# Optimization experiments

Hardware: AMD Instinct MI355X
Metric: run time of the kernel (lower is better)

Reference implementation:

```python
import jax, jax.numpy as jnp
import numpy as np

N, L, E, H = 2, 2048, 1024, 16
D = E // H  # head_dimension


def setup_inputs() -> dict:
    key = jax.random.key(0)
    kq, kk, kv, km, kw, kb = jax.random.split(key, 6)
    return {
        "query": jax.random.normal(kq, (N, L, E), dtype=jnp.float32),
        "key": jax.random.normal(kk, (N, L, E), dtype=jnp.float32),
        "value": jax.random.normal(kv, (N, L, E), dtype=jnp.float32),
        "mask": jax.random.randint(km, (N, 1, L, L), 0, 2, dtype=jnp.int32),
        "W_out": jax.random.normal(kw, (E, E), dtype=jnp.float32) / np.float32(np.sqrt(E)),
        "b_out": jax.random.normal(kb, (E,), dtype=jnp.float32) * np.float32(0.02),
    }


def reference(query, key, value, mask, W_out, b_out):
    n, ql, e = query.shape
    # split heads: [N, L, E] -> [N, L, H, D]
    q = query.reshape(n, ql, H, D)
    k = key.reshape(n, key.shape[1], H, D)
    v = value.reshape(n, value.shape[1], H, D)
    # energy: [N, H, Q, K]
    energy = jnp.einsum('nqhd,nkhd->nhqk', q, k)
    energy = jnp.where(mask == 0, jnp.float32(-1e20), energy)
    scale = jnp.float32(E) ** jnp.float32(0.5)
    attention = jax.nn.softmax(energy / scale, axis=3)
    out = jnp.einsum('nhql,nlhd->nqhd', attention, v).reshape(n, ql, H * D)
    # fully_connected_output: torch Linear -> x @ W^T + b
    return out @ W_out.T + b_out
```

## Files before the change

kernel.cpp:

```cpp
#include <hip/hip_runtime.h>
#include <hip/hip_bf16.h>

#define N_ 2
#define L_ 2048
#define E_ 1024
#define H_ 16
#define D_ 64

typedef __attribute__((ext_vector_type(8))) short bf16x8;
typedef __attribute__((ext_vector_type(4))) short bf16x4;
typedef __attribute__((ext_vector_type(4))) float f32x4;

static __device__ __forceinline__ short bfc(float f) {
    union { __bf16 h; short s; } u;
    u.h = (__bf16)f;
    return u.s;
}

static __device__ __forceinline__ void glds16(const void* g, void* l) {
    __builtin_amdgcn_global_load_lds(
        (const __attribute__((address_space(1))) unsigned int*)g,
        (__attribute__((address_space(3))) unsigned int*)l, 16, 0, 0);
}

__global__ __launch_bounds__(256) void pack_kv(
    const float* __restrict__ K, const float* __restrict__ V,
    unsigned short* __restrict__ Kp, unsigned short* __restrict__ Vp)
{
    __shared__ short T[64][72];

    const int bx = blockIdx.x;
    const int kt = bx & 31;
    const int h  = (bx >> 5) & 15;
    const int n  = bx >> 9;
    const int tid = threadIdx.x;
    const int kq = tid >> 4, c4 = tid & 15;

    const size_t inbase = ((size_t)(n * L_) + kt * 64) * E_ + h * D_;
    const size_t obase  = ((size_t)((n * H_ + h) * 32 + kt)) * 4096;

#pragma unroll
    for (int jj = 0; jj < 4; ++jj) {
        const int r = kq + jj * 16;
        const float4 f = *reinterpret_cast<const float4*>(K + inbase + (size_t)r * E_ + c4 * 4);
        bf16x4 w;
        w[0] = bfc(f.x); w[1] = bfc(f.y); w[2] = bfc(f.z); w[3] = bfc(f.w);
        *reinterpret_cast<bf16x4*>(&Kp[obase + r * 64 + ((c4 * 4) ^ ((r & 7) << 3))]) = w;
    }
#pragma unroll
    for (int jj = 0; jj < 4; ++jj) {
        const int k = kq + jj * 16;
        const float4 f = *reinterpret_cast<const float4*>(V + inbase + (size_t)k * E_ + c4 * 4);
        T[c4 * 4 + 0][k] = bfc(f.x);
        T[c4 * 4 + 1][k] = bfc(f.y);
        T[c4 * 4 + 2][k] = bfc(f.z);
        T[c4 * 4 + 3][k] = bfc(f.w);
    }
    __syncthreads();
#pragma unroll
    for (int jj = 0; jj < 2; ++jj) {
        const int d  = (tid >> 3) + jj * 32;
        const int k8 = (tid & 7) * 8;
        const bf16x8 v = *reinterpret_cast<const bf16x8*>(&T[d][k8]);
        *reinterpret_cast<bf16x8*>(&Vp[obase + d * 64 + (k8 ^ ((d & 7) << 3))]) = v;
    }
}

__global__ __launch_bounds__(256) void pack_mask(
    const int* __restrict__ mask, unsigned long long* __restrict__ Mb)
{
    const int tid  = threadIdx.x;
    const int lane = tid & 63;
    const int wave = tid >> 6;
    const int r = blockIdx.x * 4 + wave;
    const int* src = mask + (size_t)r * L_;
    unsigned long long* dst = Mb + (size_t)r * 32;
#pragma unroll 4
    for (int kt = 0; kt < 32; ++kt) {
        const int mv = src[kt * 64 + lane];
        const unsigned long long b = __ballot(mv != 0);
        if (lane == 0) dst[kt] = b;
    }
}

__global__ __launch_bounds__(256, 4) void attn_fwd(
    const unsigned short* __restrict__ Kp, const unsigned short* __restrict__ Vp,
    const float* __restrict__ Q, const unsigned long long* __restrict__ Mb,
    unsigned short* __restrict__ Obf )
{
    __shared__ __align__(16) short K_lds[2][64 * 64];
    __shared__ __align__(16) short V_lds[2][64 * 64];
    __shared__ __align__(16) short P_lds[4][32][72];

    const int tid   = threadIdx.x;
    const int lane  = tid & 63;
    const int wave  = tid >> 6;
    const int row16 = lane & 15;
    const int g     = lane >> 4;
    const int sw    = (row16 & 7) << 3;

    const int bid = blockIdx.x;
    const int bx  = (bid & 7) * 64 + (bid >> 3);
    const int qt = bx & 15;
    const int h  = (bx >> 4) & 15;
    const int n  = bx >> 8;

    const int q0w = qt * 128 + wave * 32;

    const float SCL = 0.0450842200277801f;

    bf16x8 qa[2][2];
#pragma unroll
    for (int hq = 0; hq < 2; ++hq) {
        const float* qptr = Q + ((size_t)(n * L_ + q0w + hq * 16 + row16)) * E_ + h * D_;
#pragma unroll
        for (int c = 0; c < 2; ++c) {
            const float4 f0 = *reinterpret_cast<const float4*>(qptr + 32 * c + 8 * g);
            const float4 f1 = *reinterpret_cast<const float4*>(qptr + 32 * c + 8 * g + 4);
            bf16x8 a;
            a[0] = bfc(f0.x * SCL); a[1] = bfc(f0.y * SCL);
            a[2] = bfc(f0.z * SCL); a[3] = bfc(f0.w * SCL);
            a[4] = bfc(f1.x * SCL); a[5] = bfc(f1.y * SCL);
            a[6] = bfc(f1.z * SCL); a[7] = bfc(f1.w * SCL);
            qa[hq][c] = a;
        }
    }

    f32x4 o[2][4];
#pragma unroll
    for (int hq = 0; hq < 2; ++hq)
#pragma unroll
        for (int dt = 0; dt < 4; ++dt) {
            o[hq][dt][0] = 0.f; o[hq][dt][1] = 0.f;
            o[hq][dt][2] = 0.f; o[hq][dt][3] = 0.f;
        }
    float lrun[2] = {0.f, 0.f};

    const unsigned long long* mrow0 = Mb + ((size_t)(n * L_) + q0w + row16) * 32;
    const unsigned long long* mrow1 = mrow0 + 16 * 32;
    const char* kvb = (const char*)Kp + ((size_t)(n * H_ + h) * 32) * 8192;
    const char* vvb = (const char*)Vp + ((size_t)(n * H_ + h) * 32) * 8192;

    {
        const int off = wave * 2048;
        glds16(kvb + off + lane * 16,        (char*)&K_lds[0][0] + off);
        glds16(kvb + off + 1024 + lane * 16, (char*)&K_lds[0][0] + off + 1024);
        glds16(vvb + off + lane * 16,        (char*)&V_lds[0][0] + off);
        glds16(vvb + off + 1024 + lane * 16, (char*)&V_lds[0][0] + off + 1024);
    }
    __syncthreads();

    for (int kt = 0; kt < 32; ++kt) {
        const int cur = kt & 1;
        if (kt + 1 < 32) {
            const char* kg = kvb + (size_t)(kt + 1) * 8192;
            const char* vg = vvb + (size_t)(kt + 1) * 8192;
            const int off = wave * 2048;
            glds16(kg + off + lane * 16,        (char*)&K_lds[cur ^ 1][0] + off);
            glds16(kg + off + 1024 + lane * 16, (char*)&K_lds[cur ^ 1][0] + off + 1024);
            glds16(vg + off + lane * 16,        (char*)&V_lds[cur ^ 1][0] + off);
            glds16(vg + off + 1024 + lane * 16, (char*)&V_lds[cur ^ 1][0] + off + 1024);
        }
        const unsigned long long mb0 = mrow0[kt];
        const unsigned long long mb1 = mrow1[kt];

        f32x4 s[2][4];
#pragma unroll
        for (int t = 0; t < 4; ++t) {
            f32x4 a0, a1;
            a0[0] = 0.f; a0[1] = 0.f; a0[2] = 0.f; a0[3] = 0.f;
            a1[0] = 0.f; a1[1] = 0.f; a1[2] = 0.f; a1[3] = 0.f;
#pragma unroll
            for (int c = 0; c < 2; ++c) {
                const bf16x8 kf = *reinterpret_cast<const bf16x8*>(
                    &K_lds[cur][(t * 16 + row16) * 64 + ((32 * c + 8 * g) ^ sw)]);
                a0 = __builtin_amdgcn_mfma_f32_16x16x32_bf16(kf, qa[0][c], a0, 0, 0, 0);
                a1 = __builtin_amdgcn_mfma_f32_16x16x32_bf16(kf, qa[1][c], a1, 0, 0, 0);
            }
            s[0][t] = a0; s[1][t] = a1;
        }

#pragma unroll
        for (int hq = 0; hq < 2; ++hq) {
            const unsigned long long mb = hq ? mb1 : mb0;
            const unsigned lo = (unsigned)(mb >> (g * 4));
            const unsigned hi = (unsigned)(mb >> (32 + g * 4));
            float ps = 0.f;
#pragma unroll
            for (int t = 0; t < 4; ++t) {
                const unsigned w32 = (t < 2) ? lo : hi;
                const int base = (t & 1) * 16;
#pragma unroll
                for (int i = 0; i < 4; ++i) {
                    float p = exp2f(s[hq][t][i]);
                    p = (w32 & (1u << (base + i))) ? p : 0.0f;
                    s[hq][t][i] = p;
                    ps += p;
                }
            }
            lrun[hq] += ps;
#pragma unroll
            for (int t = 0; t < 4; ++t) {
                bf16x4 w;
                w[0] = bfc(s[hq][t][0]); w[1] = bfc(s[hq][t][1]);
                w[2] = bfc(s[hq][t][2]); w[3] = bfc(s[hq][t][3]);
                *reinterpret_cast<bf16x4*>(
                    &P_lds[wave][hq * 16 + row16][(t * 16 + g * 4) ^ sw]) = w;
            }
        }

#pragma unroll
        for (int c = 0; c < 2; ++c) {
            const bf16x8 pb0 = *reinterpret_cast<const bf16x8*>(
                &P_lds[wave][row16][(32 * c + 8 * g) ^ sw]);
            const bf16x8 pb1 = *reinterpret_cast<const bf16x8*>(
                &P_lds[wave][16 + row16][(32 * c + 8 * g) ^ sw]);
#pragma unroll
            for (int dt = 0; dt < 4; ++dt) {
                const bf16x8 va = *reinterpret_cast<const bf16x8*>(
                    &V_lds[cur][(dt * 16 + row16) * 64 + ((32 * c + 8 * g) ^ sw)]);
                o[0][dt] = __builtin_amdgcn_mfma_f32_16x16x32_bf16(va, pb0, o[0][dt], 0, 0, 0);
                o[1][dt] = __builtin_amdgcn_mfma_f32_16x16x32_bf16(va, pb1, o[1][dt], 0, 0, 0);
            }
        }

        __syncthreads();
    }

#pragma unroll
    for (int hq = 0; hq < 2; ++hq) {
        float l = lrun[hq];
        l += __shfl_xor(l, 16);
        l += __shfl_xor(l, 32);
        const float inv = 1.0f / l;
        unsigned short* ob = Obf + (size_t)(n * L_ + q0w + hq * 16 + row16) * E_ + h * D_;
#pragma unroll
        for (int dt = 0; dt < 4; ++dt) {
            bf16x4 w;
            w[0] = bfc(o[hq][dt][0] * inv); w[1] = bfc(o[hq][dt][1] * inv);
            w[2] = bfc(o[hq][dt][2] * inv); w[3] = bfc(o[hq][dt][3] * inv);
            *reinterpret_cast<bf16x4*>(&ob[(dt * 16 + g * 4) ^ sw]) = w;
        }
    }
}

__global__ __launch_bounds__(256) void attn_fwd_legacy(
    const unsigned short* __restrict__ Kp, const unsigned short* __restrict__ Vp,
    const float* __restrict__ Q, const int* __restrict__ mask,
    unsigned short* __restrict__ Obf)
{
    __shared__ __align__(16) short K_lds[64 * 64];
    __shared__ __align__(16) short V_lds[64 * 64];
    __shared__ __align__(16) short P_lds[4][16][72];

    const int tid   = threadIdx.x;
    const int lane  = tid & 63;
    const int wave  = tid >> 6;
    const int row16 = lane & 15;
    const int g     = lane >> 4;
    const int sw    = (row16 & 7) << 3;

    const int bx = blockIdx.x;
    const int qt = bx & 31;
    const int h  = (bx >> 5) & 15;
    const int n  = bx >> 9;

    const int q0w = qt * 64 + wave * 16;
    const float SCL = 0.0450842200277801f;

    const float* qptr = Q + ((size_t)(n * L_ + q0w + row16)) * E_ + h * D_;
    bf16x8 qa[2];
#pragma unroll
    for (int c = 0; c < 2; ++c) {
        const float4 f0 = *reinterpret_cast<const float4*>(qptr + 32 * c + 8 * g);
        const float4 f1 = *reinterpret_cast<const float4*>(qptr + 32 * c + 8 * g + 4);
        bf16x8 a;
        a[0] = bfc(f0.x * SCL); a[1] = bfc(f0.y * SCL);
        a[2] = bfc(f0.z * SCL); a[3] = bfc(f0.w * SCL);
        a[4] = bfc(f1.x * SCL); a[5] = bfc(f1.y * SCL);
        a[6] = bfc(f1.z * SCL); a[7] = bfc(f1.w * SCL);
        qa[c] = a;
    }

    f32x4 o[4];
#pragma unroll
    for (int dt = 0; dt < 4; ++dt) { o[dt][0] = 0.f; o[dt][1] = 0.f; o[dt][2] = 0.f; o[dt][3] = 0.f; }
    float lrun = 0.f;

    const int* mrow = mask + (size_t)n * L_ * L_ + (size_t)(q0w + row16) * L_;
    const char* kvb = (const char*)Kp + ((size_t)(n * H_ + h) * 32) * 8192;
    const char* vvb = (const char*)Vp + ((size_t)(n * H_ + h) * 32) * 8192;

    for (int kt = 0; kt < 32; ++kt) {
        int4 mv[4];
#pragma unroll
        for (int t = 0; t < 4; ++t)
            mv[t] = *reinterpret_cast<const int4*>(mrow + kt * 64 + t * 16 + g * 4);

        __syncthreads();
        {
            const char* kg = kvb + (size_t)kt * 8192;
            const char* vg = vvb + (size_t)kt * 8192;
#pragma unroll
            for (int it = 0; it < 2; ++it) {
                const int off = wave * 2048 + it * 1024;
                glds16(kg + off + lane * 16, (char*)K_lds + off);
                glds16(vg + off + lane * 16, (char*)V_lds + off);
            }
        }
        __syncthreads();

        f32x4 s[4];
#pragma unroll
        for (int t = 0; t < 4; ++t) {
            f32x4 acc; acc[0] = 0.f; acc[1] = 0.f; acc[2] = 0.f; acc[3] = 0.f;
#pragma unroll
            for (int c = 0; c < 2; ++c) {
                const bf16x8 kf = *reinterpret_cast<const bf16x8*>(
                    &K_lds[(t * 16 + row16) * 64 + ((32 * c + 8 * g) ^ sw)]);
                acc = __builtin_amdgcn_mfma_f32_16x16x32_bf16(kf, qa[c], acc, 0, 0, 0);
            }
            s[t] = acc;
        }
#pragma unroll
        for (int t = 0; t < 4; ++t) {
            s[t][0] = mv[t].x ? s[t][0] : -3.0e18f;
            s[t][1] = mv[t].y ? s[t][1] : -3.0e18f;
            s[t][2] = mv[t].z ? s[t][2] : -3.0e18f;
            s[t][3] = mv[t].w ? s[t][3] : -3.0e18f;
        }
        float ps = 0.f;
#pragma unroll
        for (int t = 0; t < 4; ++t) {
            const float p0 = exp2f(s[t][0]);
            const float p1 = exp2f(s[t][1]);
            const float p2 = exp2f(s[t][2]);
            const float p3 = exp2f(s[t][3]);
            s[t][0] = p0; s[t][1] = p1; s[t][2] = p2; s[t][3] = p3;
            ps += (p0 + p1) + (p2 + p3);
        }
        lrun += ps;
#pragma unroll
        for (int t = 0; t < 4; ++t) {
            bf16x4 w;
            w[0] = bfc(s[t][0]); w[1] = bfc(s[t][1]);
            w[2] = bfc(s[t][2]); w[3] = bfc(s[t][3]);
            *reinterpret_cast<bf16x4*>(&P_lds[wave][row16][t * 16 + g * 4]) = w;
        }
#pragma unroll
        for (int c = 0; c < 2; ++c) {
            const bf16x8 pb = *reinterpret_cast<const bf16x8*>(
                &P_lds[wave][row16][32 * c + 8 * g]);
#pragma unroll
            for (int dt = 0; dt < 4; ++dt) {
                const bf16x8 va = *reinterpret_cast<const bf16x8*>(
                    &V_lds[(dt * 16 + row16) * 64 + ((32 * c + 8 * g) ^ sw)]);
                o[dt] = __builtin_amdgcn_mfma_f32_16x16x32_bf16(va, pb, o[dt], 0, 0, 0);
            }
        }
    }

    float l = lrun;
    l += __shfl_xor(l, 16);
    l += __shfl_xor(l, 32);
    const float inv = 1.0f / l;
    unsigned short* ob = Obf + (size_t)(n * L_ + q0w + row16) * E_ + h * D_;
#pragma unroll
    for (int dt = 0; dt < 4; ++dt) {
        bf16x4 w;
        w[0] = bfc(o[dt][0] * inv); w[1] = bfc(o[dt][1] * inv);
        w[2] = bfc(o[dt][2] * inv); w[3] = bfc(o[dt][3] * inv);
        *reinterpret_cast<bf16x4*>(&ob[(dt * 16 + g * 4) ^ sw]) = w;
    }
}

__global__ __launch_bounds__(256) void convert_w(
    const float* __restrict__ W, unsigned short* __restrict__ Wb)
{
    const int i = (blockIdx.x * 256 + threadIdx.x) * 4;
    const int row = i >> 10, col = i & 1023;
    const float4 f = *reinterpret_cast<const float4*>(W + i);
    bf16x4 w;
    w[0] = bfc(f.x); w[1] = bfc(f.y); w[2] = bfc(f.z); w[3] = bfc(f.w);
    const int ch = col & ~63, incol = col & 63;
    *reinterpret_cast<bf16x4*>(&Wb[row * 1024 + ch + (incol ^ ((row & 7) << 3))]) = w;
}

__global__ __launch_bounds__(256) void out_proj_bf(
    const unsigned short* __restrict__ A,
    const unsigned short* __restrict__ Wb,
    const float* __restrict__ bias, float* __restrict__ Cout)
{
    __shared__ __align__(16) short A_lds[128 * 64];
    __shared__ __align__(16) short W_lds[128 * 64];

    const int tid   = threadIdx.x;
    const int lane  = tid & 63;
    const int wave  = tid >> 6;
    const int row16 = lane & 15;
    const int g     = lane >> 4;
    const int sw    = (row16 & 7) << 3;
    const int wm = wave >> 1, wn = wave & 1;

    const int m0 = (blockIdx.x & 31) * 128;
    const int n0 = (blockIdx.x >> 5) * 128;

    f32x4 acc[4][4];
#pragma unroll
    for (int fm = 0; fm < 4; ++fm)
#pragma unroll
        for (int fn = 0; fn < 4; ++fn) {
            acc[fm][fn][0] = 0.f; acc[fm][fn][1] = 0.f;
            acc[fm][fn][2] = 0.f; acc[fm][fn][3] = 0.f;
        }

    for (int k0 = 0; k0 < 1024; k0 += 64) {
        __syncthreads();
#pragma unroll
        for (int it = 0; it < 4; ++it) {
            const int off = wave * 4096 + it * 1024;
            const int r = (off >> 7) + (lane >> 3);
            const int ib = (lane & 7) * 16;
            glds16((const char*)A + (size_t)(m0 + r) * 2048 + k0 * 2 + ib,
                   (char*)A_lds + off);
            glds16((const char*)Wb + (size_t)(n0 + r) * 2048 + k0 * 2 + ib,
                   (char*)W_lds + off);
        }
        __syncthreads();

#pragma unroll
        for (int c = 0; c < 2; ++c) {
            bf16x8 af[4], wf[4];
#pragma unroll
            for (int f = 0; f < 4; ++f) {
                af[f] = *reinterpret_cast<const bf16x8*>(
                    &A_lds[(wm * 64 + f * 16 + row16) * 64 + ((32 * c + 8 * g) ^ sw)]);
                wf[f] = *reinterpret_cast<const bf16x8*>(
                    &W_lds[(wn * 64 + f * 16 + row16) * 64 + ((32 * c + 8 * g) ^ sw)]);
            }
#pragma unroll
            for (int fm = 0; fm < 4; ++fm)
#pragma unroll
                for (int fn = 0; fn < 4; ++fn)
                    acc[fm][fn] = __builtin_amdgcn_mfma_f32_16x16x32_bf16(
                        af[fm], wf[fn], acc[fm][fn], 0, 0, 0);
        }
    }

#pragma unroll
    for (int fm = 0; fm < 4; ++fm)
#pragma unroll
        for (int fn = 0; fn < 4; ++fn) {
            const int nn = n0 + wn * 64 + fn * 16 + row16;
            const int mm = m0 + wm * 64 + fm * 16 + g * 4;
            const float b = bias[nn];
#pragma unroll
            for (int i = 0; i < 4; ++i)
                Cout[(size_t)(mm + i) * 1024 + nn] = acc[fm][fn][i] + b;
        }
}

__global__ __launch_bounds__(256) void out_proj_wf32(
    const unsigned short* __restrict__ A,
    const float* __restrict__ W,
    const float* __restrict__ bias, float* __restrict__ Cout)
{
    __shared__ __align__(16) short A_lds[128 * 64];
    __shared__ __align__(16) short W_lds[128 * 64];

    const int tid   = threadIdx.x;
    const int lane  = tid & 63;
    const int wave  = tid >> 6;
    const int row16 = lane & 15;
    const int g     = lane >> 4;
    const int sw    = (row16 & 7) << 3;
    const int wm = wave >> 1, wn = wave & 1;

    const int m0 = (blockIdx.x & 31) * 128;
    const int n0 = (blockIdx.x >> 5) * 128;

    f32x4 acc[4][4];
#pragma unroll
    for (int fm = 0; fm < 4; ++fm)
#pragma unroll
        for (int fn = 0; fn < 4; ++fn) {
            acc[fm][fn][0] = 0.f; acc[fm][fn][1] = 0.f;
            acc[fm][fn][2] = 0.f; acc[fm][fn][3] = 0.f;
        }

    for (int k0 = 0; k0 < 1024; k0 += 64) {
        __syncthreads();
#pragma unroll
        for (int it = 0; it < 4; ++it) {
            const int off = wave * 4096 + it * 1024;
            const int r = (off >> 7) + (lane >> 3);
            const int ib = (lane & 7) * 16;
            glds16((const char*)A + (size_t)(m0 + r) * 2048 + k0 * 2 + ib,
                   (char*)A_lds + off);
        }
#pragma unroll
        for (int it = 0; it < 2; ++it) {
            const int idx = tid + it * 256;
            const int r = idx >> 2, c16 = (idx & 3) * 16;
            const float* wp = W + (size_t)(n0 + r) * 1024 + k0 + c16;
            const float4 f0 = *reinterpret_cast<const float4*>(wp);
            const float4 f1 = *reinterpret_cast<const float4*>(wp + 4);
            const float4 f2 = *reinterpret_cast<const float4*>(wp + 8);
            const float4 f3 = *reinterpret_cast<const float4*>(wp + 12);
            bf16x8 w0, w1;
            w0[0] = bfc(f0.x); w0[1] = bfc(f0.y); w0[2] = bfc(f0.z); w0[3] = bfc(f0.w);
            w0[4] = bfc(f1.x); w0[5] = bfc(f1.y); w0[6] = bfc(f1.z); w0[7] = bfc(f1.w);
            w1[0] = bfc(f2.x); w1[1] = bfc(f2.y); w1[2] = bfc(f2.z); w1[3] = bfc(f2.w);
            w1[4] = bfc(f3.x); w1[5] = bfc(f3.y); w1[6] = bfc(f3.z); w1[7] = bfc(f3.w);
            const int swr = (r & 7) << 3;
            *reinterpret_cast<bf16x8*>(&W_lds[r * 64 + (c16 ^ swr)]) = w0;
            *reinterpret_cast<bf16x8*>(&W_lds[r * 64 + ((c16 + 8) ^ swr)]) = w1;
        }
        __syncthreads();

#pragma unroll
        for (int c = 0; c < 2; ++c) {
            bf16x8 af[4], wf[4];
#pragma unroll
            for (int f = 0; f < 4; ++f) {
                af[f] = *reinterpret_cast<const bf16x8*>(
                    &A_lds[(wm * 64 + f * 16 + row16) * 64 + ((32 * c + 8 * g) ^ sw)]);
                wf[f] = *reinterpret_cast<const bf16x8*>(
                    &W_lds[(wn * 64 + f * 16 + row16) * 64 + ((32 * c + 8 * g) ^ sw)]);
            }
#pragma unroll
            for (int fm = 0; fm < 4; ++fm)
#pragma unroll
                for (int fn = 0; fn < 4; ++fn)
                    acc[fm][fn] = __builtin_amdgcn_mfma_f32_16x16x32_bf16(
                        af[fm], wf[fn], acc[fm][fn], 0, 0, 0);
        }
    }

#pragma unroll
    for (int fm = 0; fm < 4; ++fm)
#pragma unroll
        for (int fn = 0; fn < 4; ++fn) {
            const int nn = n0 + wn * 64 + fn * 16 + row16;
            const int mm = m0 + wm * 64 + fm * 16 + g * 4;
            const float b = bias[nn];
#pragma unroll
            for (int i = 0; i < 4; ++i)
                Cout[(size_t)(mm + i) * 1024 + nn] = acc[fm][fn][i] + b;
        }
}

extern "C" void kernel_launch(void* const* d_in, const int* in_sizes, int n_in,
                              void* d_out, int out_size, void* d_ws, size_t ws_size,
                              hipStream_t stream) {
    const float* Q    = (const float*)d_in[0];
    const float* K    = (const float*)d_in[1];
    const float* V    = (const float*)d_in[2];
    const int*   mask = (const int*)d_in[3];
    const float* W    = (const float*)d_in[4];
    const float* b    = (const float*)d_in[5];
    float* out = (float*)d_out;

    unsigned short* Kp = (unsigned short*)d_out;
    unsigned short* Vp = (unsigned short*)d_out + (size_t)4096 * 1024;
    unsigned short* Ob = (unsigned short*)d_ws;

    const size_t MB1 = (size_t)1024 * 1024;

    pack_kv<<<dim3(1024), dim3(256), 0, stream>>>(K, V, Kp, Vp);

    if (ws_size >= 9 * MB1) {
        unsigned long long* Mbits = (unsigned long long*)((char*)d_ws + 8 * MB1);
        pack_mask<<<dim3(1024), dim3(256), 0, stream>>>(mask, Mbits);
        attn_fwd<<<dim3(512), dim3(256), 0, stream>>>(Kp, Vp, Q, Mbits, Ob);
        if (ws_size >= 11 * MB1) {
            unsigned short* Wb = (unsigned short*)((char*)d_ws + 9 * MB1);
            convert_w<<<dim3(1024), dim3(256), 0, stream>>>(W, Wb);
            out_proj_bf<<<dim3(256), dim3(256), 0, stream>>>(Ob, Wb, b, out);
        } else {
            out_proj_wf32<<<dim3(256), dim3(256), 0, stream>>>(Ob, W, b, out);
        }
    } else {
        attn_fwd_legacy<<<dim3(1024), dim3(256), 0, stream>>>(Kp, Vp, Q, mask, Ob);
        if (ws_size >= 10 * MB1) {
            unsigned short* Wb = (unsigned short*)((char*)d_ws + 8 * MB1);
            convert_w<<<dim3(1024), dim3(256), 0, stream>>>(W, Wb);
            out_proj_bf<<<dim3(256), dim3(256), 0, stream>>>(Ob, Wb, b, out);
        } else {
            out_proj_wf32<<<dim3(256), dim3(256), 0, stream>>>(Ob, W, b, out);
        }
    }
}
```

Before: 250.1 us.

## Shrink attention tiles to 16 rows per wave and double-buffer out-projection GEMM

The attention kernel now gives each wave 16 query rows instead of 32 and launches twice as many blocks (1024). This halves per-wave registers and raises occupancy, at the cost of reloading each K/V tile for more blocks. The output projection switches to 128x64 tiles with double-buffered async LDS loads and 512 blocks, so global loads overlap MFMA work. MFMA sections are wrapped in s_setprio, and the legacy kernel's P buffer gains XOR swizzling to avoid LDS bank conflicts.

```diff
diff --git a/kernel.cpp b/kernel.cpp
--- a/kernel.cpp
+++ b/kernel.cpp
@@ -90,7 +90,7 @@
 {
     __shared__ __align__(16) short K_lds[2][64 * 64];
     __shared__ __align__(16) short V_lds[2][64 * 64];
-    __shared__ __align__(16) short P_lds[4][32][72];
+    __shared__ __align__(16) short P_lds[4][16][64];
 
     const int tid   = threadIdx.x;
     const int lane  = tid & 63;
@@ -100,44 +100,35 @@
     const int sw    = (row16 & 7) << 3;
 
     const int bid = blockIdx.x;
-    const int bx  = (bid & 7) * 64 + (bid >> 3);
-    const int qt = bx & 15;
-    const int h  = (bx >> 4) & 15;
-    const int n  = bx >> 8;
-
-    const int q0w = qt * 128 + wave * 32;
+    const int bx  = (bid & 7) * 128 + (bid >> 3);
+    const int qt = bx & 31;
+    const int h  = (bx >> 5) & 15;
+    const int n  = bx >> 9;
+
+    const int q0w = qt * 64 + wave * 16;
 
     const float SCL = 0.0450842200277801f;
 
-    bf16x8 qa[2][2];
-#pragma unroll
-    for (int hq = 0; hq < 2; ++hq) {
-        const float* qptr = Q + ((size_t)(n * L_ + q0w + hq * 16 + row16)) * E_ + h * D_;
-#pragma unroll
-        for (int c = 0; c < 2; ++c) {
-            const float4 f0 = *reinterpret_cast<const float4*>(qptr + 32 * c + 8 * g);
-            const float4 f1 = *reinterpret_cast<const float4*>(qptr + 32 * c + 8 * g + 4);
-            bf16x8 a;
-            a[0] = bfc(f0.x * SCL); a[1] = bfc(f0.y * SCL);
-            a[2] = bfc(f0.z * SCL); a[3] = bfc(f0.w * SCL);
-            a[4] = bfc(f1.x * SCL); a[5] = bfc(f1.y * SCL);
-            a[6] = bfc(f1.z * SCL); a[7] = bfc(f1.w * SCL);
-            qa[hq][c] = a;
-        }
-    }
-
-    f32x4 o[2][4];
-#pragma unroll
-    for (int hq = 0; hq < 2; ++hq)
-#pragma unroll
-        for (int dt = 0; dt < 4; ++dt) {
-            o[hq][dt][0] = 0.f; o[hq][dt][1] = 0.f;
-            o[hq][dt][2] = 0.f; o[hq][dt][3] = 0.f;
-        }
-    float lrun[2] = {0.f, 0.f};
-
-    const unsigned long long* mrow0 = Mb + ((size_t)(n * L_) + q0w + row16) * 32;
-    const unsigned long long* mrow1 = mrow0 + 16 * 32;
+    const float* qptr = Q + ((size_t)(n * L_ + q0w + row16)) * E_ + h * D_;
+    bf16x8 qa[2];
+#pragma unroll
+    for (int c = 0; c < 2; ++c) {
+        const float4 f0 = *reinterpret_cast<const float4*>(qptr + 32 * c + 8 * g);
+        const float4 f1 = *reinterpret_cast<const float4*>(qptr + 32 * c + 8 * g + 4);
+        bf16x8 a;
+        a[0] = bfc(f0.x * SCL); a[1] = bfc(f0.y * SCL);
+        a[2] = bfc(f0.z * SCL); a[3] = bfc(f0.w * SCL);
+        a[4] = bfc(f1.x * SCL); a[5] = bfc(f1.y * SCL);
+        a[6] = bfc(f1.z * SCL); a[7] = bfc(f1.w * SCL);
+        qa[c] = a;
+    }
+
+    f32x4 o[4];
+#pragma unroll
+    for (int dt = 0; dt < 4; ++dt) { o[dt][0] = 0.f; o[dt][1] = 0.f; o[dt][2] = 0.f; o[dt][3] = 0.f; }
+    float lrun = 0.f;
+
+    const unsigned long long* mrow = Mb + ((size_t)(n * L_) + q0w + row16) * 32;
     const char* kvb = (const char*)Kp + ((size_t)(n * H_ + h) * 32) * 8192;
     const char* vvb = (const char*)Vp + ((size_t)(n * H_ + h) * 32) * 8192;
 
@@ -161,86 +152,77 @@
             glds16(vg + off + lane * 16,        (char*)&V_lds[cur ^ 1][0] + off);
             glds16(vg + off + 1024 + lane * 16, (char*)&V_lds[cur ^ 1][0] + off + 1024);
         }
-        const unsigned long long mb0 = mrow0[kt];
-        const unsigned long long mb1 = mrow1[kt];
-
-        f32x4 s[2][4];
+        const unsigned long long mb = mrow[kt];
+
+        f32x4 s[4];
+        __builtin_amdgcn_s_setprio(1);
 #pragma unroll
         for (int t = 0; t < 4; ++t) {
-            f32x4 a0, a1;
-            a0[0] = 0.f; a0[1] = 0.f; a0[2] = 0.f; a0[3] = 0.f;
-            a1[0] = 0.f; a1[1] = 0.f; a1[2] = 0.f; a1[3] = 0.f;
+            f32x4 acc; acc[0] = 0.f; acc[1] = 0.f; acc[2] = 0.f; acc[3] = 0.f;
 #pragma unroll
             for (int c = 0; c < 2; ++c) {
                 const bf16x8 kf = *reinterpret_cast<const bf16x8*>(
                     &K_lds[cur][(t * 16 + row16) * 64 + ((32 * c + 8 * g) ^ sw)]);
-                a0 = __builtin_amdgcn_mfma_f32_16x16x32_bf16(kf, qa[0][c], a0, 0, 0, 0);
-                a1 = __builtin_amdgcn_mfma_f32_16x16x32_bf16(kf, qa[1][c], a1, 0, 0, 0);
-            }
-            s[0][t] = a0; s[1][t] = a1;
-        }
-
-#pragma unroll
-        for (int hq = 0; hq < 2; ++hq) {
-            const unsigned long long mb = hq ? mb1 : mb0;
-            const unsigned lo = (unsigned)(mb >> (g * 4));
-            const unsigned hi = (unsigned)(mb >> (32 + g * 4));
-            float ps = 0.f;
-#pragma unroll
-            for (int t = 0; t < 4; ++t) {
-                const unsigned w32 = (t < 2) ? lo : hi;
-                const int base = (t & 1) * 16;
-#pragma unroll
-                for (int i = 0; i < 4; ++i) {
-                    float p = exp2f(s[hq][t][i]);
-                    p = (w32 & (1u << (base + i))) ? p : 0.0f;
-                    s[hq][t][i] = p;
-                    ps += p;
-                }
-            }
-            lrun[hq] += ps;
-#pragma unroll
-            for (int t = 0; t < 4; ++t) {
-                bf16x4 w;
-                w[0] = bfc(s[hq][t][0]); w[1] = bfc(s[hq][t][1]);
-                w[2] = bfc(s[hq][t][2]); w[3] = bfc(s[hq][t][3]);
-                *reinterpret_cast<bf16x4*>(
-                    &P_lds[wave][hq * 16 + row16][(t * 16 + g * 4) ^ sw]) = w;
-            }
-        }
-
+                acc = __builtin_amdgcn_mfma_f32_16x16x32_bf16(kf, qa[c], acc, 0, 0, 0);
+            }
+            s[t] = acc;
+        }
+        __builtin_amdgcn_s_setprio(0);
+
+        const unsigned lo = (unsigned)(mb >> (g * 4));
+        const unsigned hi = (unsigned)(mb >> (32 + g * 4));
+        float ps = 0.f;
+#pragma unroll
+        for (int t = 0; t < 4; ++t) {
+            const unsigned w32 = (t < 2) ? lo : hi;
+            const int base = (t & 1) * 16;
+#pragma unroll
+            for (int i = 0; i < 4; ++i) {
+                float p = exp2f(s[t][i]);
+                p = (w32 & (1u << (base + i))) ? p : 0.0f;
+                s[t][i] = p;
+                ps += p;
+            }
+        }
+        lrun += ps;
+
+#pragma unroll
+        for (int t = 0; t < 4; ++t) {
+            bf16x4 w;
+            w[0] = bfc(s[t][0]); w[1] = bfc(s[t][1]);
+            w[2] = bfc(s[t][2]); w[3] = bfc(s[t][3]);
+            *reinterpret_cast<bf16x4*>(
+                &P_lds[wave][row16][(t * 16 + g * 4) ^ sw]) = w;
+        }
+
+        __builtin_amdgcn_s_setprio(1);
 #pragma unroll
         for (int c = 0; c < 2; ++c) {
-            const bf16x8 pb0 = *reinterpret_cast<const bf16x8*>(
+            const bf16x8 pb = *reinterpret_cast<const bf16x8*>(
                 &P_lds[wave][row16][(32 * c + 8 * g) ^ sw]);
-            const bf16x8 pb1 = *reinterpret_cast<const bf16x8*>(
-                &P_lds[wave][16 + row16][(32 * c + 8 * g) ^ sw]);
 #pragma unroll
             for (int dt = 0; dt < 4; ++dt) {
                 const bf16x8 va = *reinterpret_cast<const bf16x8*>(
                     &V_lds[cur][(dt * 16 + row16) * 64 + ((32 * c + 8 * g) ^ sw)]);
-                o[0][dt] = __builtin_amdgcn_mfma_f32_16x16x32_bf16(va, pb0, o[0][dt], 0, 0, 0);
-                o[1][dt] = __builtin_amdgcn_mfma_f32_16x16x32_bf16(va, pb1, o[1][dt], 0, 0, 0);
-            }
-        }
+                o[dt] = __builtin_amdgcn_mfma_f32_16x16x32_bf16(va, pb, o[dt], 0, 0, 0);
+            }
+        }
+        __builtin_amdgcn_s_setprio(0);
 
         __syncthreads();
     }
 
-#pragma unroll
-    for (int hq = 0; hq < 2; ++hq) {
-        float l = lrun[hq];
-        l += __shfl_xor(l, 16);
-        l += __shfl_xor(l, 32);
-        const float inv = 1.0f / l;
-        unsigned short* ob = Obf + (size_t)(n * L_ + q0w + hq * 16 + row16) * E_ + h * D_;
-#pragma unroll
-        for (int dt = 0; dt < 4; ++dt) {
-            bf16x4 w;
-            w[0] = bfc(o[hq][dt][0] * inv); w[1] = bfc(o[hq][dt][1] * inv);
-            w[2] = bfc(o[hq][dt][2] * inv); w[3] = bfc(o[hq][dt][3] * inv);
-            *reinterpret_cast<bf16x4*>(&ob[(dt * 16 + g * 4) ^ sw]) = w;
-        }
+    float l = lrun;
+    l += __shfl_xor(l, 16);
+    l += __shfl_xor(l, 32);
+    const float inv = 1.0f / l;
+    unsigned short* ob = Obf + (size_t)(n * L_ + q0w + row16) * E_ + h * D_;
+#pragma unroll
+    for (int dt = 0; dt < 4; ++dt) {
+        bf16x4 w;
+        w[0] = bfc(o[dt][0] * inv); w[1] = bfc(o[dt][1] * inv);
+        w[2] = bfc(o[dt][2] * inv); w[3] = bfc(o[dt][3] * inv);
+        *reinterpret_cast<bf16x4*>(&ob[(dt * 16 + g * 4) ^ sw]) = w;
     }
 }
 
@@ -251,7 +233,7 @@
 {
     __shared__ __align__(16) short K_lds[64 * 64];
     __shared__ __align__(16) short V_lds[64 * 64];
-    __shared__ __align__(16) short P_lds[4][16][72];
+    __shared__ __align__(16) short P_lds[4][16][64];
 
     const int tid   = threadIdx.x;
     const int lane  = tid & 63;
@@ -345,12 +327,12 @@
             bf16x4 w;
             w[0] = bfc(s[t][0]); w[1] = bfc(s[t][1]);
             w[2] = bfc(s[t][2]); w[3] = bfc(s[t][3]);
-            *reinterpret_cast<bf16x4*>(&P_lds[wave][row16][t * 16 + g * 4]) = w;
+            *reinterpret_cast<bf16x4*>(&P_lds[wave][row16][(t * 16 + g * 4) ^ sw]) = w;
         }
 #pragma unroll
         for (int c = 0; c < 2; ++c) {
             const bf16x8 pb = *reinterpret_cast<const bf16x8*>(
-                &P_lds[wave][row16][32 * c + 8 * g]);
+                &P_lds[wave][row16][(32 * c + 8 * g) ^ sw]);
 #pragma unroll
             for (int dt = 0; dt < 4; ++dt) {
                 const bf16x8 va = *reinterpret_cast<const bf16x8*>(
@@ -386,13 +368,13 @@
     *reinterpret_cast<bf16x4*>(&Wb[row * 1024 + ch + (incol ^ ((row & 7) << 3))]) = w;
 }
 
-__global__ __launch_bounds__(256) void out_proj_bf(
-    const unsigned short* __restrict__ A,
-    const unsigned short* __restrict__ Wb,
+__global__ __launch_bounds__(256, 4) void out_proj_bf(
+    const unsigned short* __restrict__ A ,
+    const unsigned short* __restrict__ Wb ,
     const float* __restrict__ bias, float* __restrict__ Cout)
 {
-    __shared__ __align__(16) short A_lds[128 * 64];
-    __shared__ __align__(16) short W_lds[128 * 64];
+    __shared__ __align__(16) short A_lds[2][128 * 64];
+    __shared__ __align__(16) short W_lds[2][64 * 64];
 
     const int tid   = threadIdx.x;
     const int lane  = tid & 63;
@@ -400,59 +382,90 @@
     const int row16 = lane & 15;
     const int g     = lane >> 4;
     const int sw    = (row16 & 7) << 3;
-    const int wm = wave >> 1, wn = wave & 1;
-
-    const int m0 = (blockIdx.x & 31) * 128;
-    const int n0 = (blockIdx.x >> 5) * 128;
-
-    f32x4 acc[4][4];
-#pragma unroll
-    for (int fm = 0; fm < 4; ++fm)
+
+    const int bid = blockIdx.x;
+    const int bx  = (bid & 7) * 64 + (bid >> 3);
+    const int m0 = (bx & 31) * 128;
+    const int n0 = (bx >> 5) * 64;
+
+    const int ib = (lane & 7) * 16;
+    const int rl = lane >> 3;
+
+    f32x4 acc[2][4];
+#pragma unroll
+    for (int fm = 0; fm < 2; ++fm)
 #pragma unroll
         for (int fn = 0; fn < 4; ++fn) {
             acc[fm][fn][0] = 0.f; acc[fm][fn][1] = 0.f;
             acc[fm][fn][2] = 0.f; acc[fm][fn][3] = 0.f;
         }
 
-    for (int k0 = 0; k0 < 1024; k0 += 64) {
-        __syncthreads();
+    {
 #pragma unroll
         for (int it = 0; it < 4; ++it) {
             const int off = wave * 4096 + it * 1024;
-            const int r = (off >> 7) + (lane >> 3);
-            const int ib = (lane & 7) * 16;
-            glds16((const char*)A + (size_t)(m0 + r) * 2048 + k0 * 2 + ib,
-                   (char*)A_lds + off);
-            glds16((const char*)Wb + (size_t)(n0 + r) * 2048 + k0 * 2 + ib,
-                   (char*)W_lds + off);
-        }
-        __syncthreads();
-
+            const int r = (off >> 7) + rl;
+            glds16((const char*)A + (size_t)(m0 + r) * 2048 + ib, (char*)&A_lds[0][0] + off);
+        }
+#pragma unroll
+        for (int it = 0; it < 2; ++it) {
+            const int off = wave * 2048 + it * 1024;
+            const int r = (off >> 7) + rl;
+            glds16((const char*)Wb + (size_t)(n0 + r) * 2048 + ib, (char*)&W_lds[0][0] + off);
+        }
+    }
+    __syncthreads();
+
+    for (int kk = 0; kk < 16; ++kk) {
+        const int cur = kk & 1;
+        if (kk + 1 < 16) {
+            const int kb = (kk + 1) * 128;
+#pragma unroll
+            for (int it = 0; it < 4; ++it) {
+                const int off = wave * 4096 + it * 1024;
+                const int r = (off >> 7) + rl;
+                glds16((const char*)A + (size_t)(m0 + r) * 2048 + kb + ib,
+                       (char*)&A_lds[cur ^ 1][0] + off);
+            }
+#pragma unroll
+            for (int it = 0; it < 2; ++it) {
+                const int off = wave * 2048 + it * 1024;
+                const int r = (off >> 7) + rl;
+                glds16((const char*)Wb + (size_t)(n0 + r) * 2048 + kb + ib,
+                       (char*)&W_lds[cur ^ 1][0] + off);
+            }
+        }
+
+        __builtin_amdgcn_s_setprio(1);
 #pragma unroll
         for (int c = 0; c < 2; ++c) {
-            bf16x8 af[4], wf[4];
-#pragma unroll
-            for (int f = 0; f < 4; ++f) {
-                af[f] = *reinterpret_cast<const bf16x8*>(
-                    &A_lds[(wm * 64 + f * 16 + row16) * 64 + ((32 * c + 8 * g) ^ sw)]);
-                wf[f] = *reinterpret_cast<const bf16x8*>(
-                    &W_lds[(wn * 64 + f * 16 + row16) * 64 + ((32 * c + 8 * g) ^ sw)]);
-            }
-#pragma unroll
-            for (int fm = 0; fm < 4; ++fm)
+            bf16x8 af[2], wf[4];
+#pragma unroll
+            for (int fm = 0; fm < 2; ++fm)
+                af[fm] = *reinterpret_cast<const bf16x8*>(
+                    &A_lds[cur][(wave * 32 + fm * 16 + row16) * 64 + ((32 * c + 8 * g) ^ sw)]);
+#pragma unroll
+            for (int fn = 0; fn < 4; ++fn)
+                wf[fn] = *reinterpret_cast<const bf16x8*>(
+                    &W_lds[cur][(fn * 16 + row16) * 64 + ((32 * c + 8 * g) ^ sw)]);
+#pragma unroll
+            for (int fm = 0; fm < 2; ++fm)
 #pragma unroll
                 for (int fn = 0; fn < 4; ++fn)
                     acc[fm][fn] = __builtin_amdgcn_mfma_f32_16x16x32_bf16(
                         af[fm], wf[fn], acc[fm][fn], 0, 0, 0);
         }
-    }
-
-#pragma unroll
-    for (int fm = 0; fm < 4; ++fm)
+        __builtin_amdgcn_s_setprio(0);
+
+        __syncthreads();
+    }
+
+#pragma unroll
+    for (int fm = 0; fm < 2; ++fm)
 #pragma unroll
         for (int fn = 0; fn < 4; ++fn) {
-            const int nn = n0 + wn * 64 + fn * 16 + row16;
-            const int mm = m0 + wm * 64 + fm * 16 + g * 4;
+            const int nn = n0 + fn * 16 + row16;
+            const int mm = m0 + wave * 32 + fm * 16 + g * 4;
             const float b = bias[nn];
 #pragma unroll
             for (int i = 0; i < 4; ++i)
@@ -572,11 +585,11 @@
     if (ws_size >= 9 * MB1) {
         unsigned long long* Mbits = (unsigned long long*)((char*)d_ws + 8 * MB1);
         pack_mask<<<dim3(1024), dim3(256), 0, stream>>>(mask, Mbits);
-        attn_fwd<<<dim3(512), dim3(256), 0, stream>>>(Kp, Vp, Q, Mbits, Ob);
+        attn_fwd<<<dim3(1024), dim3(256), 0, stream>>>(Kp, Vp, Q, Mbits, Ob);
         if (ws_size >= 11 * MB1) {
             unsigned short* Wb = (unsigned short*)((char*)d_ws + 9 * MB1);
             convert_w<<<dim3(1024), dim3(256), 0, stream>>>(W, Wb);
-            out_proj_bf<<<dim3(256), dim3(256), 0, stream>>>(Ob, Wb, b, out);
+            out_proj_bf<<<dim3(512), dim3(256), 0, stream>>>(Ob, Wb, b, out);
         } else {
             out_proj_wf32<<<dim3(256), dim3(256), 0, stream>>>(Ob, W, b, out);
         }
@@ -585,7 +598,7 @@
         if (ws_size >= 10 * MB1) {
             unsigned short* Wb = (unsigned short*)((char*)d_ws + 8 * MB1);
             convert_w<<<dim3(1024), dim3(256), 0, stream>>>(W, Wb);
-            out_proj_bf<<<dim3(256), dim3(256), 0, stream>>>(Ob, Wb, b, out);
+            out_proj_bf<<<dim3(512), dim3(256), 0, stream>>>(Ob, Wb, b, out);
         } else {
             out_proj_wf32<<<dim3(256), dim3(256), 0, stream>>>(Ob, W, b, out);
         }
```

Measured after the change: 226.3 us. -9.5%, faster.
